# Optimization experiments

Measured on AMD Instinct MI355X. Metric: run time of the kernel, lower is better.

The kernel has to match this reference:

```python
import jax, jax.numpy as jnp
import numpy as np

B, T, D, H, DK = 4, 2048, 1024, 16, 64
DV = 2 * DK
QKD = H * DK           # 1024
VD = H * DV            # 2048
KW = 4                 # conv kernel size
EPS = 1e-5


def zc_rms(x, scale):
    # zero-centered RMS norm over last axis
    xc = x - jnp.mean(x, axis=-1, keepdims=True)
    return xc * jax.lax.rsqrt(jnp.mean(xc * xc, axis=-1, keepdims=True) + EPS) * scale


def causal_dwconv(x, kern, bias):
    # depthwise causal conv1d: x [B,T,C], kern [K,C], bias [C]
    k = kern.shape[0]
    t = x.shape[1]
    xp = jnp.pad(x, ((0, 0), (k - 1, 0), (0, 0)))
    out = bias
    for i in range(k):  # small fixed K=4
        out = out + xp[:, i:i + t, :] * kern[i]
    return out


def _forward(x, q_w, k_w, v_w, q_scale, k_scale, v_scale,
             q_conv_k, q_conv_b, k_conv_k, k_conv_b, v_conv_k, v_conv_b,
             alpha_w, beta_w, out_w, gate_w):
    # Q/K/V: Dense -> zero-centered RMSNorm -> causal depthwise conv -> SiLU
    q = jax.nn.silu(causal_dwconv(zc_rms(x @ q_w, q_scale), q_conv_k, q_conv_b))
    k = jax.nn.silu(causal_dwconv(zc_rms(x @ k_w, k_scale), k_conv_k, k_conv_b))
    v = jax.nn.silu(causal_dwconv(zc_rms(x @ v_w, v_scale), v_conv_k, v_conv_b))

    q = q.reshape(B, T, H, DK)
    k = k.reshape(B, T, H, DK)
    v = v.reshape(B, T, H, DV)

    alpha = jax.nn.sigmoid(x @ alpha_w)  # [B,T,H] per-head decay gate
    beta = jax.nn.sigmoid(x @ beta_w)    # [B,T,H] per-head write strength

    def step(S, inp):
        # S: [B,H,DK,DV]
        qt, kt, vt, at, bt = inp
        Sd = at[..., None, None] * S                              # gated decay
        pred = jnp.einsum('bhd,bhdv->bhv', kt, Sd)                # current memory readout at k
        S_new = Sd + bt[..., None, None] * jnp.einsum('bhd,bhv->bhdv', kt, vt - pred)  # delta rule
        ot = jnp.einsum('bhd,bhdv->bhv', qt, S_new)
        return S_new, ot

    xs = (jnp.transpose(q, (1, 0, 2, 3)),
          jnp.transpose(k, (1, 0, 2, 3)),
          jnp.transpose(v, (1, 0, 2, 3)),
          jnp.transpose(alpha, (1, 0, 2)),
          jnp.transpose(beta, (1, 0, 2)))
    S0 = jnp.zeros((B, H, DK, DV), x.dtype)
    _, o = jax.lax.scan(step, S0, xs)                             # o: [T,B,H,DV]

    core = jnp.transpose(o, (1, 0, 2, 3)).reshape(B, T, VD)
    # gated linear unit output
    return (core @ out_w) * jax.nn.sigmoid(x @ gate_w)


def setup_inputs() -> dict:
    key = jax.random.key(0)
    ks = jax.random.split(key, 12)
    g = lambda i, shape, s: jax.random.normal(ks[i], shape, dtype=jnp.float32) * s
    return {
        'x': g(0, (B, T, D), 1.0),
        'q_w': g(1, (D, QKD), 0.02), 'k_w': g(2, (D, QKD), 0.02), 'v_w': g(3, (D, VD), 0.02),
        'q_scale': jnp.ones((QKD,), jnp.float32),
        'k_scale': jnp.ones((QKD,), jnp.float32),
        'v_scale': jnp.ones((VD,), jnp.float32),
        'q_conv_k': g(4, (KW, QKD), 0.1), 'q_conv_b': jnp.zeros((QKD,), jnp.float32),
        'k_conv_k': g(5, (KW, QKD), 0.1), 'k_conv_b': jnp.zeros((QKD,), jnp.float32),
        'v_conv_k': g(6, (KW, VD), 0.1), 'v_conv_b': jnp.zeros((VD,), jnp.float32),
        'alpha_w': g(7, (D, H), 0.02), 'beta_w': g(8, (D, H), 0.02),
        'out_w': g(9, (VD, D), 0.02), 'gate_w': g(10, (D, D), 0.02),
    }


def reference(x, q_w, k_w, v_w, q_scale, k_scale, v_scale,
              q_conv_k, q_conv_b, k_conv_k, k_conv_b, v_conv_k, v_conv_b,
              alpha_w, beta_w, out_w, gate_w):
    return _forward(x, q_w, k_w, v_w, q_scale, k_scale, v_scale,
                    q_conv_k, q_conv_b, k_conv_k, k_conv_b, v_conv_k, v_conv_b,
                    alpha_w, beta_w, out_w, gate_w)
```

## Files before the change

### kernel.cpp

```cpp
#include <hip/hip_runtime.h>

#define Bc   4
#define Tc   2048
#define Dc   1024
#define Hc   16
#define DKc  64
#define DVc  128
#define QKDc 1024
#define VDc  2048
#define NPRJ 5120
#define Mc   (Bc * Tc)
#define CHUNK 64
#define NCHK (Tc / CHUNK)

typedef __bf16 bf16;
typedef __bf16 bf16x4 __attribute__((ext_vector_type(4)));
typedef __bf16 bf16x8 __attribute__((ext_vector_type(8)));
typedef float  f32x4  __attribute__((ext_vector_type(4)));

__device__ __forceinline__ float bf2f(bf16 v) { return (float)v; }
__device__ __forceinline__ bf16  f2bf(float v) { return (bf16)v; }
__device__ __forceinline__ float sigmoidf_(float x) { return 1.0f / (1.0f + __expf(-x)); }
__device__ __forceinline__ f32x4 mfma16(bf16x8 a, bf16x8 b, f32x4 c) {
    return __builtin_amdgcn_mfma_f32_16x16x32_bf16(a, b, c, 0, 0, 0);
}

__device__ __forceinline__ void glds16(const bf16* g, void* l) {
    __builtin_amdgcn_global_load_lds((const __attribute__((address_space(1))) void*)g,
                                     (__attribute__((address_space(3))) void*)l, 16, 0, 0);
}

__device__ __forceinline__ bf16* swz32x64(bf16* base, int r, int k) {
    int byte = (((r << 6) + k) << 1) ^ ((r & 7) << 4);
    return (bf16*)((char*)base + byte);
}

__global__ __launch_bounds__(256) void cast_f32_bf16(const float* __restrict__ src,
                                                     bf16* __restrict__ dst, int n4) {
    int i = blockIdx.x * 256 + threadIdx.x;
    if (i < n4) {
        float4 v = ((const float4*)src)[i];
        bf16x4 o = { f2bf(v.x), f2bf(v.y), f2bf(v.z), f2bf(v.w) };
        ((bf16x4*)dst)[i] = o;
    }
}

__global__ __launch_bounds__(256) void transpose_cast(const float* __restrict__ src,
                                                      bf16* __restrict__ dst,
                                                      int R, int C) {
    __shared__ float tile[32][33];
    int c0 = blockIdx.x * 32, r0 = blockIdx.y * 32;
    int tx = threadIdx.x, ty = threadIdx.y;
#pragma unroll
    for (int i = 0; i < 32; i += 8) {
        int r = r0 + ty + i, c = c0 + tx;
        tile[ty + i][tx] = (r < R && c < C) ? src[(size_t)r * C + c] : 0.0f;
    }
    __syncthreads();
#pragma unroll
    for (int i = 0; i < 32; i += 8) {
        int rr = c0 + ty + i, cc = r0 + tx;
        if (rr < C && cc < R) dst[(size_t)rr * R + cc] = f2bf(tile[tx][ty + i]);
    }
}

#define GP_NT 20
#define GP_MT 32
#define GP_NKT 32
__global__ __launch_bounds__(512) void gemm_pipe(const bf16* __restrict__ A,
                                                 const bf16* __restrict__ Bt,
                                                 bf16* __restrict__ C) {
    __shared__ __align__(16) char lds[131072];
    const int tid = threadIdx.x;
    const int wid = tid >> 6, lane = tid & 63;
    const int lm = lane & 15, lq = lane >> 4;
    const int wm = wid >> 2, wn = wid & 3;

    const int id = blockIdx.x;
    const int nid = (id & 7) * ((GP_NT * GP_MT) / 8) + (id >> 3);
    const int tn = nid % GP_NT, tm = nid / GP_NT;
    const int n0 = tn * 256, m0 = tm * 256;

    const int r0 = tid >> 2;
    const int lsx = ((tid & 3) ^ (r0 & 3)) << 3;
    const bf16* sA0 = A  + (size_t)(m0 + r0) * Dc + lsx;
    const bf16* sA1 = sA0 + (size_t)128 * Dc;
    const bf16* sB0 = Bt + (size_t)(n0 + r0) * Dc + lsx;
    const bf16* sB1 = sB0 + (size_t)128 * Dc;

    auto stageA = [&](int kt) {
        char* d = lds + ((kt & 3) << 15) + wid * 1024;
        glds16(sA0 + kt * 32, d);
        glds16(sA1 + kt * 32, d + 8192);
    };
    auto stageB = [&](int kt) {
        char* d = lds + ((kt & 3) << 15) + 16384 + wid * 1024;
        glds16(sB0 + kt * 32, d);
        glds16(sB1 + kt * 32, d + 8192);
    };

    f32x4 acc[8][4] = {};
    const int sx = (lq ^ (lm & 3)) << 3;
    const int aoff = wm * 4096 + lm * 32 + sx;
    const int boff = wn * 2048 + lm * 32 + sx;

    stageA(0); stageB(0); stageA(1); stageB(1);
    asm volatile("s_waitcnt vmcnt(4)" ::: "memory");
    asm volatile("s_barrier" ::: "memory");

    for (int kt = 0; kt < GP_NKT; kt++) {
        const bf16* sA = (const bf16*)(lds + ((kt & 3) << 15));
        const bf16* sB = (const bf16*)(lds + ((kt & 3) << 15) + 16384);
        bf16x8 aF[4], bF[4], aG[4];
#pragma unroll
        for (int i = 0; i < 4; i++) aF[i] = *(const bf16x8*)&sA[aoff + i * 512];
#pragma unroll
        for (int j = 0; j < 4; j++) bF[j] = *(const bf16x8*)&sB[boff + j * 512];
        if (kt + 2 < GP_NKT) stageA(kt + 2);
        asm volatile("s_waitcnt lgkmcnt(0)" ::: "memory");
        __builtin_amdgcn_sched_barrier(0);
        __builtin_amdgcn_s_setprio(1);
#pragma unroll
        for (int i = 0; i < 4; i++)
#pragma unroll
            for (int j = 0; j < 4; j++)
                acc[i][j] = mfma16(aF[i], bF[j], acc[i][j]);
        __builtin_amdgcn_s_setprio(0);
#pragma unroll
        for (int i = 0; i < 4; i++) aG[i] = *(const bf16x8*)&sA[aoff + (i + 4) * 512];
        if (kt + 2 < GP_NKT) stageB(kt + 2);
        asm volatile("s_waitcnt lgkmcnt(0)" ::: "memory");
        __builtin_amdgcn_sched_barrier(0);
        __builtin_amdgcn_s_setprio(1);
#pragma unroll
        for (int i = 0; i < 4; i++)
#pragma unroll
            for (int j = 0; j < 4; j++)
                acc[i + 4][j] = mfma16(aG[i], bF[j], acc[i + 4][j]);
        __builtin_amdgcn_s_setprio(0);
        if (kt + 2 < GP_NKT) asm volatile("s_waitcnt vmcnt(4)" ::: "memory");
        else                 asm volatile("s_waitcnt vmcnt(0)" ::: "memory");
        asm volatile("s_barrier" ::: "memory");
    }

    const int rbase = m0 + wm * 128 + lq * 4;
    const int cbase = n0 + wn * 64 + lm;
#pragma unroll
    for (int i = 0; i < 8; i++)
#pragma unroll
        for (int j = 0; j < 4; j++)
#pragma unroll
            for (int rI = 0; rI < 4; rI++)
                C[(size_t)(rbase + i * 16 + rI) * NPRJ + cbase + j * 16] =
                    f2bf(acc[i][j][rI]);
}

template <typename OutT>
__global__ __launch_bounds__(256) void gemm_bt(const bf16* __restrict__ A,
                                               const bf16* __restrict__ Bt,
                                               OutT* __restrict__ C,
                                               int M, int N, int K,
                                               const bf16* __restrict__ gate,
                                               int lda, int ldc, int ldg) {
    __shared__ bf16 As[128 * 32];
    __shared__ bf16 Bs[128 * 32];

    const int n0 = blockIdx.x * 128;
    const int m0 = blockIdx.y * 128;
    const int t = threadIdx.x;
    const int wid = t >> 6, lane = t & 63;
    const int wm = (wid & 1) * 64;
    const int wn = (wid >> 1) * 64;

    f32x4 acc[4][4] = {};

    const int srow = lane >> 2;
    const int scol = (lane & 3) * 8;
    char* AsB = (char*)As;
    char* BsB = (char*)Bs;

    for (int k0 = 0; k0 < K; k0 += 32) {
        glds16(&A[(size_t)(m0 + wid * 16 + srow) * lda + k0 + scol],       AsB + wid * 1024);
        glds16(&A[(size_t)(m0 + 64 + wid * 16 + srow) * lda + k0 + scol],  AsB + 4096 + wid * 1024);
        glds16(&Bt[(size_t)(n0 + wid * 16 + srow) * K + k0 + scol],        BsB + wid * 1024);
        glds16(&Bt[(size_t)(n0 + 64 + wid * 16 + srow) * K + k0 + scol],   BsB + 4096 + wid * 1024);
        __syncthreads();

        const int kh = (lane >> 4) * 8;
        const int lm = lane & 15;
        bf16x8 a[4], b[4];
#pragma unroll
        for (int i = 0; i < 4; i++) a[i] = *(const bf16x8*)&As[(wm + i * 16 + lm) * 32 + kh];
#pragma unroll
        for (int j = 0; j < 4; j++) b[j] = *(const bf16x8*)&Bs[(wn + j * 16 + lm) * 32 + kh];
#pragma unroll
        for (int i = 0; i < 4; i++)
#pragma unroll
            for (int j = 0; j < 4; j++)
                acc[i][j] = __builtin_amdgcn_mfma_f32_16x16x32_bf16(a[i], b[j], acc[i][j], 0, 0, 0);
        __syncthreads();
    }

    const int lm = lane & 15, lq = lane >> 4;
#pragma unroll
    for (int i = 0; i < 4; i++) {
#pragma unroll
        for (int j = 0; j < 4; j++) {
#pragma unroll
            for (int rI = 0; rI < 4; rI++) {
                int row = m0 + wm + i * 16 + lq * 4 + rI;
                int col = n0 + wn + j * 16 + lm;
                float val = acc[i][j][rI];
                if (gate) {
                    float g = bf2f(gate[(size_t)row * ldg + col]);
                    val *= sigmoidf_(g);
                }
                C[(size_t)row * ldc + col] = (OutT)val;
            }
        }
    }
}

template <int L>
__global__ __launch_bounds__(256) void zc_rms_kernel(bf16* __restrict__ buf,
                                                     const float* __restrict__ scale,
                                                     int ld) {
    constexpr int NPT = L / 256;
    int row = blockIdx.x;
    int t = threadIdx.x;
    bf16* p = buf + (size_t)row * ld;

    float xv[NPT];
    float s = 0.f, s2 = 0.f;
#pragma unroll
    for (int i = 0; i < NPT; i++) {
        float x = bf2f(p[t + (i << 8)]);
        xv[i] = x;
        s += x;
        s2 += x * x;
    }
    __shared__ float red[2][4];
#pragma unroll
    for (int o = 32; o > 0; o >>= 1) {
        s += __shfl_down(s, o, 64);
        s2 += __shfl_down(s2, o, 64);
    }
    if ((t & 63) == 0) { red[0][t >> 6] = s; red[1][t >> 6] = s2; }
    __syncthreads();
    s  = red[0][0] + red[0][1] + red[0][2] + red[0][3];
    s2 = red[1][0] + red[1][1] + red[1][2] + red[1][3];

    float mean = s / (float)L;
    float var = s2 / (float)L - mean * mean;
    float inv = rsqrtf(var + 1e-5f);
#pragma unroll
    for (int i = 0; i < NPT; i++) {
        float y = (xv[i] - mean) * inv * scale[t + (i << 8)];
        p[t + (i << 8)] = f2bf(y);
    }
}

__global__ __launch_bounds__(256) void conv_silu(const bf16* __restrict__ xn,
                                                 const float* __restrict__ kern,
                                                 const float* __restrict__ bias,
                                                 bf16* __restrict__ out,
                                                 int Cch, int ldin) {
    int btok = blockIdx.x;
    int tt = btok & (Tc - 1);
    for (int c = threadIdx.x; c < Cch; c += 256) {
        float acc = bias[c];
#pragma unroll
        for (int i = 0; i < 4; i++) {
            int ts = tt - 3 + i;
            if (ts >= 0)
                acc += bf2f(xn[(size_t)(btok - 3 + i) * ldin + c]) * kern[i * Cch + c];
        }
        float y = acc * sigmoidf_(acc);
        out[(size_t)btok * Cch + c] = f2bf(y);
    }
}

__global__ __launch_bounds__(256) void alphabeta_mfma(const bf16* __restrict__ x,
                                                      const float* __restrict__ aw,
                                                      const float* __restrict__ bw,
                                                      float* __restrict__ af,
                                                      float* __restrict__ bfv) {
    __shared__ bf16 whi[32][136];
    __shared__ bf16 wlo[32][136];
    const int tid = threadIdx.x, wave = tid >> 6, lane = tid & 63;
    const int lm = lane & 15, lq = lane >> 4;
    const int m0 = blockIdx.x * 128;
    f32x4 acc[2][2] = {};

    for (int k0 = 0; k0 < Dc; k0 += 128) {
        for (int idx = tid; idx < 4096; idx += 256) {
            int n = idx & 31, kk = idx >> 5;
            float v = (n < 16) ? aw[(size_t)(k0 + kk) * Hc + n]
                               : bw[(size_t)(k0 + kk) * Hc + (n - 16)];
            bf16 h = f2bf(v);
            whi[n][kk] = h;
            wlo[n][kk] = f2bf(v - bf2f(h));
        }
        __syncthreads();
#pragma unroll
        for (int ks = 0; ks < 4; ks++) {
            bf16x8 bh[2], bl[2];
#pragma unroll
            for (int j = 0; j < 2; j++) {
                bh[j] = *(const bf16x8*)&whi[j * 16 + lm][ks * 32 + lq * 8];
                bl[j] = *(const bf16x8*)&wlo[j * 16 + lm][ks * 32 + lq * 8];
            }
#pragma unroll
            for (int ii = 0; ii < 2; ii++) {
                int row = m0 + wave * 32 + ii * 16 + lm;
                bf16x8 a = *(const bf16x8*)&x[(size_t)row * Dc + k0 + ks * 32 + lq * 8];
#pragma unroll
                for (int j = 0; j < 2; j++) {
                    acc[ii][j] = mfma16(a, bh[j], acc[ii][j]);
                    acc[ii][j] = mfma16(a, bl[j], acc[ii][j]);
                }
            }
        }
        __syncthreads();
    }
#pragma unroll
    for (int ii = 0; ii < 2; ii++)
#pragma unroll
        for (int rI = 0; rI < 4; rI++) {
            int row = m0 + wave * 32 + ii * 16 + lq * 4 + rI;
            af[(size_t)row * Hc + lm]  = sigmoidf_(acc[ii][0][rI]);
            bfv[(size_t)row * Hc + lm] = sigmoidf_(acc[ii][1][rI]);
        }
}

__global__ __launch_bounds__(256) void prep(bf16* __restrict__ qf,
                                            bf16* __restrict__ kf,
                                            bf16* __restrict__ vc,
                                            const float* __restrict__ af,
                                            const float* __restrict__ bfv,
                                            bf16* __restrict__ Wb,
                                            bf16* __restrict__ Mb,
                                            float* __restrict__ gamC) {
    __shared__ __align__(16) char smem[53248];
    bf16*  Kc   = (bf16*)(smem);
    bf16*  Qc   = (bf16*)(smem + 9216);
    float* DT   = (float*)(smem + 9216);
    float* Pn   = (float*)(smem + 13568);
    float* TT   = (float*)(smem + 15744);
    float* Qn   = (float*)(smem + 9216);
    bf16*  Tb   = (bf16*)(smem + 9216);
    float* As   = (float*)(smem + 18432);
    bf16*  Vtb  = (bf16*)(smem + 18432);
    float* Ts   = (float*)(smem + 35072);
    float* lg_s = (float*)(smem + 51712);
    float* bv_s = lg_s + 64;
    float* bg_s = lg_s + 128;
    float* gm_s = lg_s + 192;
    float* kr_s = lg_s + 256;

    const int c    = blockIdx.x;
    const int bh   = blockIdx.y;
    const int b    = bh >> 4, h = bh & 15;
    const int ch   = bh * NCHK + c;
    const int tok0 = b * Tc + c * CHUNK;
    const int tid  = threadIdx.x;
    const int wave = tid >> 6, lane = tid & 63;
    const int lm = lane & 15, lq = lane >> 4, kh = lq * 8;

#pragma unroll
    for (int r = 0; r < 2; r++) {
        int idx = tid + r * 256;
        int row = idx >> 3, c8 = (idx & 7) * 8;
        *(bf16x8*)&Kc[row * 72 + c8] =
            *(const bf16x8*)&kf[(size_t)(tok0 + row) * QKDc + h * DKc + c8];
        *(bf16x8*)&Qc[row * 72 + c8] =
            *(const bf16x8*)&qf[(size_t)(tok0 + row) * QKDc + h * DKc + c8];
    }
    for (int idx = tid; idx < 64 * 65; idx += 256) Ts[idx] = 0.f;
    if (tid < 64) {
        float a  = af[(size_t)(tok0 + tid) * Hc + h];
        float bb = bfv[(size_t)(tok0 + tid) * Hc + h];
        float la = __log2f(fmaxf(a, 1e-30f));
#pragma unroll
        for (int o = 1; o < 64; o <<= 1) {
            float t = __shfl_up(la, o, 64);
            if (tid >= o) la += t;
        }
        float lgC = __shfl(la, 63, 64);
        lg_s[tid] = la;
        bv_s[tid] = bb;
        float g   = exp2f(la);
        gm_s[tid] = g;
        bg_s[tid] = bb * g;
        kr_s[tid] = exp2f(lgC - la);
        if (tid == 0) gamC[ch] = exp2f(lgC);
    }
    __syncthreads();

    {
        bf16x8 ka[2], qa[2];
#pragma unroll
        for (int s = 0; s < 2; s++) {
            ka[s] = *(const bf16x8*)&Kc[(16 * wave + lm) * 72 + s * 32 + kh];
            qa[s] = *(const bf16x8*)&Qc[(16 * wave + lm) * 72 + s * 32 + kh];
        }
#pragma unroll
        for (int jt = 0; jt < 4; jt++) {
            f32x4 kkacc = {}, qkacc = {};
#pragma unroll
            for (int s = 0; s < 2; s++) {
                bf16x8 kbf = *(const bf16x8*)&Kc[(16 * jt + lm) * 72 + s * 32 + kh];
                kkacc = mfma16(ka[s], kbf, kkacc);
                qkacc = mfma16(qa[s], kbf, qkacc);
            }
#pragma unroll
            for (int rI = 0; rI < 4; rI++) {
                int i = 16 * wave + lq * 4 + rI;
                int j = 16 * jt + lm;
                float ratio = exp2f(lg_s[i] - lg_s[j]);
                As[i * 65 + j] = (j < i) ? bv_s[i] * ratio * kkacc[rI] : 0.f;
                Mb[((size_t)ch * 64 + i) * 64 + j] =
                    (j <= i) ? f2bf(ratio * qkacc[rI]) : f2bf(0.f);
            }
        }
    }
    {
#pragma unroll
        for (int r = 0; r < 2; r++) {
            int idx = tid + r * 256;
            int row = idx >> 3, c8 = (idx & 7) * 8;
            bf16x8 v = *(const bf16x8*)&Qc[row * 72 + c8];
            float g = gm_s[row];
            bf16x8 oq;
#pragma unroll
            for (int e = 0; e < 8; e++) oq[e] = f2bf(bf2f(v[e]) * g);
            *(bf16x8*)&qf[(size_t)(tok0 + row) * QKDc + h * DKc + c8] = oq;
            bf16x8 ok;
#pragma unroll
            for (int e = 0; e < 8; e++)
                ok[e] = f2bf(kr_s[c8 + e] * bf2f(Kc[(c8 + e) * 72 + row]));
            *(bf16x8*)&kf[(size_t)(tok0 + row) * QKDc + h * DKc + c8] = ok;
        }
    }
    __syncthreads();

    if (tid < 64) {
        const int g = lane >> 4, jj = lane & 15, base = lane & 48;
        float areg[16], tcol[16];
#pragma unroll
        for (int i = 0; i < 16; i++) areg[i] = As[(16 * g + i) * 65 + 16 * g + jj];
#pragma unroll
        for (int i = 0; i < 16; i++) tcol[i] = (i == jj) ? 1.f : 0.f;
#pragma unroll
        for (int i = 1; i < 16; i++) {
            float s = 0.f;
#pragma unroll
            for (int m = 0; m < i; m++)
                s = fmaf(__shfl(areg[i], base + m, 64), tcol[m], s);
            tcol[i] = (i == jj) ? 1.f : -s;
        }
#pragma unroll
        for (int i = 0; i < 16; i++) {
            Ts[(16 * g + i) * 65 + 16 * g + jj] = tcol[i];
            DT[g * 272 + jj * 17 + i] = tcol[i];
        }
    }
    __syncthreads();

    if (wave < 2) {
        const int w = wave;
        bf16x8 ah, al, bh, bl;
#pragma unroll
        for (int e = 0; e < 8; e++) {
            int k = kh + e;
            float xa = (k < 16) ? DT[2 * w * 272 + lm * 17 + k] : 0.f;
            bf16 ha = f2bf(xa); ah[e] = ha; al[e] = f2bf(xa - bf2f(ha));
            float xb = (k < 16) ? As[(16 + 32 * w + lm) * 65 + 32 * w + k] : 0.f;
            bf16 hb = f2bf(xb); bh[e] = hb; bl[e] = f2bf(xb - bf2f(hb));
        }
        f32x4 acc = {};
        acc = mfma16(ah, bh, acc); acc = mfma16(ah, bl, acc); acc = mfma16(al, bh, acc);
#pragma unroll
        for (int rI = 0; rI < 4; rI++)
            Pn[w * 272 + (lq * 4 + rI) * 17 + lm] = -acc[rI];
    }
    __syncthreads();

    if (wave < 3) {
        bf16x8 ah, al, bh, bl;
#pragma unroll
        for (int e = 0; e < 8; e++) {
            int k = kh + e;
            float xa = 0.f, xb = 0.f;
            if (k < 16) {
                if (wave == 0)      { xa = Ts[(16 + lm) * 65 + 16 + k]; xb = Pn[lm * 17 + k]; }
                else if (wave == 1) { xa = Pn[lm * 17 + k];             xb = Ts[(16 + lm) * 65 + 16 + k]; }
                else                { xa = Ts[(48 + lm) * 65 + 48 + k]; xb = Pn[272 + lm * 17 + k]; }
            }
            bf16 ha = f2bf(xa); ah[e] = ha; al[e] = f2bf(xa - bf2f(ha));
            bf16 hb = f2bf(xb); bh[e] = hb; bl[e] = f2bf(xb - bf2f(hb));
        }
        f32x4 acc = {};
        acc = mfma16(ah, bh, acc); acc = mfma16(ah, bl, acc); acc = mfma16(al, bh, acc);
#pragma unroll
        for (int rI = 0; rI < 4; rI++) {
            int ro = lq * 4 + rI;
            if (wave == 0)      Ts[(16 + ro) * 65 + lm]      = acc[rI];
            else if (wave == 1) TT[ro * 17 + lm]             = acc[rI];
            else                Ts[(48 + ro) * 65 + 32 + lm] = acc[rI];
        }
    }
    __syncthreads();

    {
        const int a = wave >> 1, bq = wave & 1;
        bf16x8 ah, al, bh, bl;
#pragma unroll
        for (int e = 0; e < 8; e++) {
            int k = kh + e;
            float xa;
            if (a == 0) xa = (k < 16) ? DT[lm * 17 + k] : TT[lm * 17 + (k - 16)];
            else        xa = (k < 16) ? 0.f : DT[272 + lm * 17 + (k - 16)];
            bf16 ha = f2bf(xa); ah[e] = ha; al[e] = f2bf(xa - bf2f(ha));
            float xb = As[(32 + 16 * bq + lm) * 65 + k];
            bf16 hb = f2bf(xb); bh[e] = hb; bl[e] = f2bf(xb - bf2f(hb));
        }
        f32x4 acc = {};
        acc = mfma16(ah, bh, acc); acc = mfma16(ah, bl, acc); acc = mfma16(al, bh, acc);
        __syncthreads();
#pragma unroll
        for (int rI = 0; rI < 4; rI++)
            Qn[(16 * a + lq * 4 + rI) * 33 + 16 * bq + lm] = -acc[rI];
    }
    __syncthreads();

    {
        const int a = wave >> 1, bq = wave & 1;
        bf16x8 ah, al, bh, bl;
#pragma unroll
        for (int e = 0; e < 8; e++) {
            int k = kh + e;
            float xa = Ts[(32 + 16 * a + lm) * 65 + 32 + k];
            bf16 ha = f2bf(xa); ah[e] = ha; al[e] = f2bf(xa - bf2f(ha));
            float xb = Qn[(16 * bq + lm) * 33 + k];
            bf16 hb = f2bf(xb); bh[e] = hb; bl[e] = f2bf(xb - bf2f(hb));
        }
        f32x4 acc = {};
        acc = mfma16(ah, bh, acc); acc = mfma16(ah, bl, acc); acc = mfma16(al, bh, acc);
#pragma unroll
        for (int rI = 0; rI < 4; rI++)
            Ts[(32 + 16 * a + lq * 4 + rI) * 65 + 16 * bq + lm] = acc[rI];
    }
    __syncthreads();

    for (int idx = tid; idx < 4096; idx += 256) {
        int i = idx >> 6, j = idx & 63;
        Tb[i * 72 + j] = f2bf(Ts[i * 65 + j]);
    }
    __syncthreads();
#pragma unroll
    for (int r = 0; r < 4; r++) {
        int idx = tid + r * 256;
        int j = idx >> 4, c8 = (idx & 15) * 8;
        bf16x8 v = *(const bf16x8*)&vc[(size_t)(tok0 + j) * VDc + h * DVc + c8];
        float bb = bv_s[j];
#pragma unroll
        for (int e = 0; e < 8; e++)
            Vtb[(c8 + e) * 72 + j] = f2bf(bf2f(v[e]) * bb);
    }
    __syncthreads();
    {
        bf16x8 ta[2];
#pragma unroll
        for (int s = 0; s < 2; s++)
            ta[s] = *(const bf16x8*)&Tb[(16 * wave + lm) * 72 + s * 32 + kh];
#pragma unroll
        for (int dt = 0; dt < 4; dt++) {
            f32x4 wacc = {};
#pragma unroll
            for (int s = 0; s < 2; s++) {
                bf16x8 wbf;
                int d = 16 * dt + lm;
#pragma unroll
                for (int e = 0; e < 8; e++) {
                    int j = s * 32 + kh + e;
                    wbf[e] = f2bf(bg_s[j] * bf2f(Kc[j * 72 + d]));
                }
                wacc = mfma16(ta[s], wbf, wacc);
            }
#pragma unroll
            for (int rI = 0; rI < 4; rI++) {
                int i = 16 * wave + lq * 4 + rI;
                Wb[((size_t)ch * 64 + i) * 64 + 16 * dt + lm] = f2bf(wacc[rI]);
            }
        }
#pragma unroll
        for (int dt = 0; dt < 8; dt++) {
            f32x4 uacc = {};
#pragma unroll
            for (int s = 0; s < 2; s++) {
                bf16x8 vb = *(const bf16x8*)&Vtb[(16 * dt + lm) * 72 + s * 32 + kh];
                uacc = mfma16(ta[s], vb, uacc);
            }
#pragma unroll
            for (int rI = 0; rI < 4; rI++) {
                int i = 16 * wave + lq * 4 + rI;
                vc[(size_t)(tok0 + i) * VDc + h * DVc + 16 * dt + lm] = f2bf(uacc[rI]);
            }
        }
    }
}

__global__ __launch_bounds__(256) void chunkloop(const bf16* __restrict__ qf,
                                                 const bf16* __restrict__ kf,
                                                 const bf16* __restrict__ vc,
                                                 const bf16* __restrict__ Wb,
                                                 const bf16* __restrict__ Mb,
                                                 const float* __restrict__ gamC,
                                                 bf16* __restrict__ o, int ldo) {
    const int vg = blockIdx.x;
    const int bh = blockIdx.y;
    const int b = bh >> 4, h = bh & 15;
    const int tid = threadIdx.x;
    const int wave = tid >> 6, lane = tid & 63;
    const int lm = lane & 15, lq = lane >> 4, kh = lq * 8;

    __shared__ __align__(16) bf16 SbBuf[32 * 64];
    __shared__ __align__(16) bf16 UtBuf[32 * 64];

    for (int idx = tid; idx < 32 * 64; idx += 256) SbBuf[idx] = f2bf(0.f);

    f32x4 Sacc[2] = {};

    const int colK = h * DKc;
    const int colV = h * DVc + vg * 32;

    bf16x8 wa[2], qa[2], ma[2], kb[2];
    bf16 uvv[2][4];

    auto loadFrags = [&](int c, bf16x8 (&wa_)[2], bf16x8 (&qa_)[2], bf16x8 (&ma_)[2],
                         bf16x8 (&kb_)[2], bf16 (&uvv_)[2][4]) {
        const int tok0 = b * Tc + c * CHUNK;
        const size_t chb = ((size_t)bh * NCHK + c) * 64;
#pragma unroll
        for (int s = 0; s < 2; s++) {
            wa_[s] = *(const bf16x8*)&Wb[(chb + 16 * wave + lm) * 64 + s * 32 + kh];
            ma_[s] = *(const bf16x8*)&Mb[(chb + 16 * wave + lm) * 64 + s * 32 + kh];
            qa_[s] = *(const bf16x8*)&qf[(size_t)(tok0 + 16 * wave + lm) * QKDc + colK + s * 32 + kh];
            kb_[s] = *(const bf16x8*)&kf[(size_t)(tok0 + 16 * wave + lm) * QKDc + colK + s * 32 + kh];
        }
#pragma unroll
        for (int dt = 0; dt < 2; dt++)
#pragma unroll
            for (int rI = 0; rI < 4; rI++)
                uvv_[dt][rI] =
                    vc[(size_t)(tok0 + 16 * wave + lq * 4 + rI) * VDc + colV + 16 * dt + lm];
    };

    loadFrags(0, wa, qa, ma, kb, uvv);
    __syncthreads();

    for (int c = 0; c < NCHK; c++) {
        const float gC = gamC[(size_t)bh * NCHK + c];
        bf16x8 sf[2][2];
#pragma unroll
        for (int dt = 0; dt < 2; dt++)
#pragma unroll
            for (int s = 0; s < 2; s++)
                sf[dt][s] = *(const bf16x8*)swz32x64(SbBuf, 16 * dt + lm, s * 32 + kh);
        f32x4 pacc[2] = {};
#pragma unroll
        for (int dt = 0; dt < 2; dt++)
#pragma unroll
            for (int s = 0; s < 2; s++)
                pacc[dt] = mfma16(wa[s], sf[dt][s], pacc[dt]);

        bf16x8 wa2[2], qa2[2], ma2[2], kb2[2];
        bf16 uvv2[2][4];
        if (c + 1 < NCHK) loadFrags(c + 1, wa2, qa2, ma2, kb2, uvv2);

#pragma unroll
        for (int dt = 0; dt < 2; dt++)
#pragma unroll
            for (int rI = 0; rI < 4; rI++) {
                float u = bf2f(uvv[dt][rI]) - pacc[dt][rI];
                *swz32x64(UtBuf, 16 * dt + lm, 16 * wave + lq * 4 + rI) = f2bf(u);
            }
        __syncthreads();

        bf16x8 uf[2][2];
#pragma unroll
        for (int dt = 0; dt < 2; dt++)
#pragma unroll
            for (int s = 0; s < 2; s++)
                uf[dt][s] = *(const bf16x8*)swz32x64(UtBuf, 16 * dt + lm, s * 32 + kh);

        f32x4 oacc[2] = {};
#pragma unroll
        for (int dt = 0; dt < 2; dt++)
#pragma unroll
            for (int s = 0; s < 2; s++) {
                oacc[dt] = mfma16(qa[s], sf[dt][s], oacc[dt]);
                oacc[dt] = mfma16(ma[s], uf[dt][s], oacc[dt]);
            }
        {
            const int tok0 = b * Tc + c * CHUNK;
#pragma unroll
            for (int dt = 0; dt < 2; dt++)
#pragma unroll
                for (int rI = 0; rI < 4; rI++)
                    o[(size_t)(tok0 + 16 * wave + lq * 4 + rI) * ldo + colV + 16 * dt + lm] =
                        f2bf(oacc[dt][rI]);
        }
#pragma unroll
        for (int dt = 0; dt < 2; dt++) {
#pragma unroll
            for (int e = 0; e < 4; e++) Sacc[dt][e] *= gC;
#pragma unroll
            for (int s = 0; s < 2; s++)
                Sacc[dt] = mfma16(uf[dt][s], kb[s], Sacc[dt]);
        }
        __syncthreads();
#pragma unroll
        for (int dt = 0; dt < 2; dt++)
#pragma unroll
            for (int rI = 0; rI < 4; rI++)
                *swz32x64(SbBuf, 16 * dt + lq * 4 + rI, 16 * wave + lm) = f2bf(Sacc[dt][rI]);
        __syncthreads();

        if (c + 1 < NCHK) {
#pragma unroll
            for (int s = 0; s < 2; s++) { wa[s] = wa2[s]; qa[s] = qa2[s]; ma[s] = ma2[s]; kb[s] = kb2[s]; }
#pragma unroll
            for (int dt = 0; dt < 2; dt++)
#pragma unroll
                for (int rI = 0; rI < 4; rI++) uvv[dt][rI] = uvv2[dt][rI];
        }
    }
}

extern "C" void kernel_launch(void* const* d_in, const int* in_sizes, int n_in,
                              void* d_out, int out_size, void* d_ws, size_t ws_size,
                              hipStream_t stream) {
    const float* x        = (const float*)d_in[0];
    const float* q_w      = (const float*)d_in[1];
    const float* k_w      = (const float*)d_in[2];
    const float* v_w      = (const float*)d_in[3];
    const float* q_scale  = (const float*)d_in[4];
    const float* k_scale  = (const float*)d_in[5];
    const float* v_scale  = (const float*)d_in[6];
    const float* q_conv_k = (const float*)d_in[7];
    const float* q_conv_b = (const float*)d_in[8];
    const float* k_conv_k = (const float*)d_in[9];
    const float* k_conv_b = (const float*)d_in[10];
    const float* v_conv_k = (const float*)d_in[11];
    const float* v_conv_b = (const float*)d_in[12];
    const float* alpha_w  = (const float*)d_in[13];
    const float* beta_w   = (const float*)d_in[14];
    const float* out_w    = (const float*)d_in[15];
    const float* gate_w   = (const float*)d_in[16];

    char* w = (char*)d_ws;
    bf16* xb  = (bf16*)w; w += (size_t)Mc * Dc * 2;
    bf16* qwT = (bf16*)w; w += (size_t)QKDc * Dc * 2;
    bf16* kwT = (bf16*)w; w += (size_t)QKDc * Dc * 2;
    bf16* vwT = (bf16*)w; w += (size_t)VDc * Dc * 2;
    bf16* gwT = (bf16*)w; w += (size_t)Dc * Dc * 2;
    bf16* owT = (bf16*)w; w += (size_t)Dc * VDc * 2;
    bf16* lin_all = (bf16*)w; w += (size_t)Mc * NPRJ * 2;
    bf16* qf = (bf16*)w; w += (size_t)Mc * QKDc * 2;
    bf16* kf = (bf16*)w; w += (size_t)Mc * QKDc * 2;
    bf16* vc = (bf16*)w; w += (size_t)Mc * VDc * 2;
    float* af = (float*)w; w += (size_t)Mc * Hc * 4;
    float* bfv = (float*)w; w += (size_t)Mc * Hc * 4;
    const int NCH_TOT = Bc * Hc * NCHK;
    bf16* Wb = (bf16*)w; w += (size_t)NCH_TOT * 64 * 64 * 2;
    bf16* Mb = (bf16*)w; w += (size_t)NCH_TOT * 64 * 64 * 2;
    float* gamC = (float*)w; w += (size_t)NCH_TOT * 4;
    bf16* o_core = lin_all;

    dim3 tb(32, 8);
    cast_f32_bf16<<<(Mc * Dc / 4 + 255) / 256, 256, 0, stream>>>(x, xb, Mc * Dc / 4);
    transpose_cast<<<dim3(QKDc / 32, Dc / 32), tb, 0, stream>>>(q_w, qwT, Dc, QKDc);
    transpose_cast<<<dim3(QKDc / 32, Dc / 32), tb, 0, stream>>>(k_w, kwT, Dc, QKDc);
    transpose_cast<<<dim3(VDc / 32, Dc / 32), tb, 0, stream>>>(v_w, vwT, Dc, VDc);
    transpose_cast<<<dim3(Dc / 32, Dc / 32), tb, 0, stream>>>(gate_w, gwT, Dc, Dc);
    transpose_cast<<<dim3(Dc / 32, VDc / 32), tb, 0, stream>>>(out_w, owT, VDc, Dc);

    gemm_pipe<<<GP_NT * GP_MT, 512, 0, stream>>>(xb, qwT, lin_all);

    zc_rms_kernel<QKDc><<<Mc, 256, 0, stream>>>(lin_all,        q_scale, NPRJ);
    zc_rms_kernel<QKDc><<<Mc, 256, 0, stream>>>(lin_all + 1024, k_scale, NPRJ);
    zc_rms_kernel<VDc><<<Mc, 256, 0, stream>>>(lin_all + 2048,  v_scale, NPRJ);

    conv_silu<<<Mc, 256, 0, stream>>>(lin_all,        q_conv_k, q_conv_b, qf, QKDc, NPRJ);
    conv_silu<<<Mc, 256, 0, stream>>>(lin_all + 1024, k_conv_k, k_conv_b, kf, QKDc, NPRJ);
    conv_silu<<<Mc, 256, 0, stream>>>(lin_all + 2048, v_conv_k, v_conv_b, vc, VDc, NPRJ);

    alphabeta_mfma<<<Mc / 128, 256, 0, stream>>>(xb, alpha_w, beta_w, af, bfv);

    prep<<<dim3(NCHK, Bc * Hc), 256, 0, stream>>>(qf, kf, vc, af, bfv, Wb, Mb, gamC);
    chunkloop<<<dim3(4, Bc * Hc), 256, 0, stream>>>(qf, kf, vc, Wb, Mb, gamC, o_core, NPRJ);

    gemm_bt<float><<<dim3(Dc / 128, Mc / 128), 256, 0, stream>>>(
        o_core, owT, (float*)d_out, Mc, Dc, VDc, lin_all + 4096, NPRJ, Dc, NPRJ);
}
```

Before: 616.2 us.

## Vectorize RMS-norm and conv kernels, add intra-iteration barriers to projection GEMM

The zero-centered RMS norm and the causal depthwise conv+SiLU kernels are rewritten so each thread handles 8 contiguous channels with 16-byte bf16x8 loads/stores and float4 parameter loads, launching L/8 threads per row instead of 256. The intent is to cut per-element memory instructions and improve coalescing on these bandwidth-bound passes. Separately, the fused projection GEMM gets launch_bounds(512,2) and extra s_barrier calls between the LDS fragment reads, async global-to-LDS staging and MFMA phases, meant to keep waves in lockstep. The extra barriers add sync overhead, and the occupancy hint may increase register pressure. A 64KB... note: 128KB LDS per block makes 2 blocks/CU unreachable, so the launch_bounds hint mostly constrains registers.

```diff
diff --git a/kernel.cpp b/kernel.cpp
--- a/kernel.cpp
+++ b/kernel.cpp
@@ -67,9 +67,9 @@
 #define GP_NT 20
 #define GP_MT 32
 #define GP_NKT 32
-__global__ __launch_bounds__(512) void gemm_pipe(const bf16* __restrict__ A,
-                                                 const bf16* __restrict__ Bt,
-                                                 bf16* __restrict__ C) {
+__global__ __launch_bounds__(512, 2) void gemm_pipe(const bf16* __restrict__ A,
+                                                    const bf16* __restrict__ Bt,
+                                                    bf16* __restrict__ C) {
     __shared__ __align__(16) char lds[131072];
     const int tid = threadIdx.x;
     const int wid = tid >> 6, lane = tid & 63;
@@ -106,7 +106,7 @@
 
     stageA(0); stageB(0); stageA(1); stageB(1);
     asm volatile("s_waitcnt vmcnt(4)" ::: "memory");
-    asm volatile("s_barrier" ::: "memory");
+    __builtin_amdgcn_s_barrier();
 
     for (int kt = 0; kt < GP_NKT; kt++) {
         const bf16* sA = (const bf16*)(lds + ((kt & 3) << 15));
@@ -117,6 +117,7 @@
 #pragma unroll
         for (int j = 0; j < 4; j++) bF[j] = *(const bf16x8*)&sB[boff + j * 512];
         if (kt + 2 < GP_NKT) stageA(kt + 2);
+        __builtin_amdgcn_s_barrier();
         asm volatile("s_waitcnt lgkmcnt(0)" ::: "memory");
         __builtin_amdgcn_sched_barrier(0);
         __builtin_amdgcn_s_setprio(1);
@@ -126,9 +127,11 @@
             for (int j = 0; j < 4; j++)
                 acc[i][j] = mfma16(aF[i], bF[j], acc[i][j]);
         __builtin_amdgcn_s_setprio(0);
+        __builtin_amdgcn_s_barrier();
 #pragma unroll
         for (int i = 0; i < 4; i++) aG[i] = *(const bf16x8*)&sA[aoff + (i + 4) * 512];
         if (kt + 2 < GP_NKT) stageB(kt + 2);
+        __builtin_amdgcn_s_barrier();
         asm volatile("s_waitcnt lgkmcnt(0)" ::: "memory");
         __builtin_amdgcn_sched_barrier(0);
         __builtin_amdgcn_s_setprio(1);
@@ -140,7 +143,7 @@
         __builtin_amdgcn_s_setprio(0);
         if (kt + 2 < GP_NKT) asm volatile("s_waitcnt vmcnt(4)" ::: "memory");
         else                 asm volatile("s_waitcnt vmcnt(0)" ::: "memory");
-        asm volatile("s_barrier" ::: "memory");
+        __builtin_amdgcn_s_barrier();
     }
 
     const int rbase = m0 + wm * 128 + lq * 4;
@@ -222,24 +225,17 @@
 }
 
 template <int L>
-__global__ __launch_bounds__(256) void zc_rms_kernel(bf16* __restrict__ buf,
-                                                     const float* __restrict__ scale,
-                                                     int ld) {
-    constexpr int NPT = L / 256;
-    int row = blockIdx.x;
-    int t = threadIdx.x;
+__global__ __launch_bounds__(256) void zc_rms_v(bf16* __restrict__ buf,
+                                                const float* __restrict__ scale,
+                                                int ld) {
+    constexpr int NW = L / 8 / 64;
+    const int row = blockIdx.x, t = threadIdx.x;
     bf16* p = buf + (size_t)row * ld;
-
-    float xv[NPT];
-    float s = 0.f, s2 = 0.f;
-#pragma unroll
-    for (int i = 0; i < NPT; i++) {
-        float x = bf2f(p[t + (i << 8)]);
-        xv[i] = x;
-        s += x;
-        s2 += x * x;
-    }
-    __shared__ float red[2][4];
+    bf16x8 v = *(const bf16x8*)&p[t * 8];
+    float xv[8], s = 0.f, s2 = 0.f;
+#pragma unroll
+    for (int e = 0; e < 8; e++) { xv[e] = bf2f(v[e]); s += xv[e]; s2 += xv[e] * xv[e]; }
+    __shared__ float red[2][NW];
 #pragma unroll
     for (int o = 32; o > 0; o >>= 1) {
         s += __shfl_down(s, o, 64);
@@ -247,37 +243,48 @@
     }
     if ((t & 63) == 0) { red[0][t >> 6] = s; red[1][t >> 6] = s2; }
     __syncthreads();
-    s  = red[0][0] + red[0][1] + red[0][2] + red[0][3];
-    s2 = red[1][0] + red[1][1] + red[1][2] + red[1][3];
-
+    s = 0.f; s2 = 0.f;
+#pragma unroll
+    for (int wv = 0; wv < NW; wv++) { s += red[0][wv]; s2 += red[1][wv]; }
     float mean = s / (float)L;
-    float var = s2 / (float)L - mean * mean;
-    float inv = rsqrtf(var + 1e-5f);
-#pragma unroll
-    for (int i = 0; i < NPT; i++) {
-        float y = (xv[i] - mean) * inv * scale[t + (i << 8)];
-        p[t + (i << 8)] = f2bf(y);
-    }
-}
-
-__global__ __launch_bounds__(256) void conv_silu(const bf16* __restrict__ xn,
-                                                 const float* __restrict__ kern,
-                                                 const float* __restrict__ bias,
-                                                 bf16* __restrict__ out,
-                                                 int Cch, int ldin) {
-    int btok = blockIdx.x;
-    int tt = btok & (Tc - 1);
-    for (int c = threadIdx.x; c < Cch; c += 256) {
-        float acc = bias[c];
-#pragma unroll
-        for (int i = 0; i < 4; i++) {
-            int ts = tt - 3 + i;
-            if (ts >= 0)
-                acc += bf2f(xn[(size_t)(btok - 3 + i) * ldin + c]) * kern[i * Cch + c];
-        }
-        float y = acc * sigmoidf_(acc);
-        out[(size_t)btok * Cch + c] = f2bf(y);
-    }
+    float inv = rsqrtf(s2 / (float)L - mean * mean + 1e-5f);
+    float4 s0 = *(const float4*)&scale[t * 8];
+    float4 s1 = *(const float4*)&scale[t * 8 + 4];
+    float sc[8] = { s0.x, s0.y, s0.z, s0.w, s1.x, s1.y, s1.z, s1.w };
+    bf16x8 o;
+#pragma unroll
+    for (int e = 0; e < 8; e++) o[e] = f2bf((xv[e] - mean) * inv * sc[e]);
+    *(bf16x8*)&p[t * 8] = o;
+}
+
+template <int CCH>
+__global__ __launch_bounds__(256) void conv_silu_v(const bf16* __restrict__ xn,
+                                                   const float* __restrict__ kern,
+                                                   const float* __restrict__ bias,
+                                                   bf16* __restrict__ out, int ldin) {
+    const int btok = blockIdx.x;
+    const int tt = btok & (Tc - 1);
+    const int c8 = threadIdx.x * 8;
+    float4 b0 = *(const float4*)&bias[c8], b1 = *(const float4*)&bias[c8 + 4];
+    float acc[8] = { b0.x, b0.y, b0.z, b0.w, b1.x, b1.y, b1.z, b1.w };
+#pragma unroll
+    for (int i = 0; i < 4; i++) {
+        if (tt - 3 + i >= 0) {
+            bf16x8 xv = *(const bf16x8*)&xn[(size_t)(btok - 3 + i) * ldin + c8];
+            float4 k0 = *(const float4*)&kern[i * CCH + c8];
+            float4 k1 = *(const float4*)&kern[i * CCH + c8 + 4];
+            float kk[8] = { k0.x, k0.y, k0.z, k0.w, k1.x, k1.y, k1.z, k1.w };
+#pragma unroll
+            for (int e = 0; e < 8; e++) acc[e] += bf2f(xv[e]) * kk[e];
+        }
+    }
+    bf16x8 o;
+#pragma unroll
+    for (int e = 0; e < 8; e++) {
+        float y = acc[e] * sigmoidf_(acc[e]);
+        o[e] = f2bf(y);
+    }
+    *(bf16x8*)&out[(size_t)btok * CCH + c8] = o;
 }
 
 __global__ __launch_bounds__(256) void alphabeta_mfma(const bf16* __restrict__ x,
@@ -789,13 +796,13 @@
 
     gemm_pipe<<<GP_NT * GP_MT, 512, 0, stream>>>(xb, qwT, lin_all);
 
-    zc_rms_kernel<QKDc><<<Mc, 256, 0, stream>>>(lin_all,        q_scale, NPRJ);
-    zc_rms_kernel<QKDc><<<Mc, 256, 0, stream>>>(lin_all + 1024, k_scale, NPRJ);
-    zc_rms_kernel<VDc><<<Mc, 256, 0, stream>>>(lin_all + 2048,  v_scale, NPRJ);
-
-    conv_silu<<<Mc, 256, 0, stream>>>(lin_all,        q_conv_k, q_conv_b, qf, QKDc, NPRJ);
-    conv_silu<<<Mc, 256, 0, stream>>>(lin_all + 1024, k_conv_k, k_conv_b, kf, QKDc, NPRJ);
-    conv_silu<<<Mc, 256, 0, stream>>>(lin_all + 2048, v_conv_k, v_conv_b, vc, VDc, NPRJ);
+    zc_rms_v<QKDc><<<Mc, QKDc / 8, 0, stream>>>(lin_all,        q_scale, NPRJ);
+    zc_rms_v<QKDc><<<Mc, QKDc / 8, 0, stream>>>(lin_all + 1024, k_scale, NPRJ);
+    zc_rms_v<VDc><<<Mc, VDc / 8, 0, stream>>>(lin_all + 2048,   v_scale, NPRJ);
+
+    conv_silu_v<QKDc><<<Mc, QKDc / 8, 0, stream>>>(lin_all,        q_conv_k, q_conv_b, qf, NPRJ);
+    conv_silu_v<QKDc><<<Mc, QKDc / 8, 0, stream>>>(lin_all + 1024, k_conv_k, k_conv_b, kf, NPRJ);
+    conv_silu_v<VDc><<<Mc, VDc / 8, 0, stream>>>(lin_all + 2048,   v_conv_k, v_conv_b, vc, NPRJ);
 
     alphabeta_mfma<<<Mc / 128, 256, 0, stream>>>(xb, alpha_w, beta_w, af, bfv);
 
```

Result: faster. 562.6 us (-8.7%).
